# Optimization experiments

Hardware: AMD Instinct MI355X
Metric: run time of the kernel (lower is better)

Reference implementation:

```python
import jax, jax.numpy as jnp
import numpy as np

B, L, D = 2, 2048, 1024
H = 16
C = 128            # chunk_size
N = L // C         # num chunks
SCALE = float(np.sqrt(D))  # softmax_scale = sqrt(d_model)


def setup_inputs() -> dict:
    key = jax.random.key(0)
    ks = jax.random.split(key, 5)
    return {
        "x": jax.random.normal(ks[0], (B, L, D), dtype=jnp.float32),
        "w_qkv": jax.random.normal(ks[1], (D, 3 * D), dtype=jnp.float32) * (1.0 / np.sqrt(D)),
        "b_qkv": jax.random.normal(ks[2], (3 * D,), dtype=jnp.float32) * 0.02,
        "w_o": jax.random.normal(ks[3], (D, D), dtype=jnp.float32) * (1.0 / np.sqrt(D)),
        "b_o": jax.random.normal(ks[4], (D,), dtype=jnp.float32) * 0.02,
    }


def reference(x, w_qkv, b_qkv, w_o, b_o):
    b, l, d = x.shape
    hd = d // H
    qkv = x @ w_qkv + b_qkv                         # (B,L,3D)
    q, k, v = jnp.split(qkv, 3, axis=-1)
    q = q.reshape(b, l, H, hd)
    k = k.reshape(b, l, H, hd)
    v = v.reshape(b, l, H, hd)

    q_chunks = q.reshape(b, N, C, H, hd)
    k_chunks = k.reshape(b, N, C, H, hd)
    # mean_pool over the chunk dim
    q_pool = q_chunks.mean(axis=2)                  # (B,N,H,hd)
    k_pool = k_chunks.mean(axis=2)

    token2chunk = jnp.einsum('blhd,bnhd->bhln', q, k_pool)          # (B,H,L,N)
    chunk2token = jnp.einsum('bnhd,bnchd->bhnc', q_pool, k_chunks)  # (B,H,N,C)
    # outer product over (n,c) -> full (B,H,L,L) score matrix
    A = token2chunk[..., :, None] * chunk2token[:, :, None, :, :]   # (B,H,L,N,C)
    A = A.reshape(b, H, l, l)

    # direct intra-chunk attention overwrites the diagonal blocks
    direct = jnp.einsum('bnqhd,bnkhd->bhnqk', q_chunks, k_chunks)   # (B,H,N,C,C)
    A6 = A.reshape(b, H, N, C, N, C)
    eye = jnp.eye(N, dtype=bool)[:, None, :, None]                  # (N,1,N,1)
    A6 = jnp.where(eye, direct[:, :, :, :, None, :], A6)
    A = A6.reshape(b, H, l, l)

    # causal mask applied multiplicatively (masked scores become 0, NOT -inf)
    causal = jnp.tril(jnp.ones((l, l), dtype=bool))
    A = jnp.where(causal, A, 0.0) / SCALE
    A = jax.nn.softmax(A, axis=-1)

    out = jnp.einsum('bhqv,bvhd->bhqd', A, v)       # (B,H,L,hd)
    out = out.transpose(0, 2, 1, 3).reshape(b, l, d)
    return out @ w_o + b_o
```

## Files before the change

kernel.cpp:

```cpp
#include <hip/hip_runtime.h>
#include <math.h>

#define B_   2
#define L_   2048
#define D_   1024
#define H_   16
#define HD_  64
#define C_   128
#define N_   16
#define INV_SCALE 0.03125f
#define SCL2 0.0450842200f

typedef _Float16 h8 __attribute__((ext_vector_type(8)));
typedef _Float16 h4 __attribute__((ext_vector_type(4)));
typedef float    f4 __attribute__((ext_vector_type(4)));

#define MFMA16(a, b, c) __builtin_amdgcn_mfma_f32_16x16x32_f16((a), (b), (c), 0, 0, 0)

#if __has_builtin(__builtin_amdgcn_exp2f)
#define EXP2(x) __builtin_amdgcn_exp2f(x)
#else
#define EXP2(x) exp2f(x)
#endif

__device__ __forceinline__ void gl_lds16(const void* g, void* l) {
  __builtin_amdgcn_global_load_lds(
      (const __attribute__((address_space(1))) void*)g,
      (__attribute__((address_space(3))) void*)l, 16, 0, 0);
}

#define SBAR()  do { __builtin_amdgcn_sched_barrier(0); \
                     __builtin_amdgcn_s_barrier();      \
                     __builtin_amdgcn_sched_barrier(0); } while (0)
#define LGKM0() do { asm volatile("s_waitcnt lgkmcnt(0)" ::: "memory"); \
                     __builtin_amdgcn_sched_barrier(0); } while (0)
#define VMW(n)  do { asm volatile("s_waitcnt vmcnt(" #n ")" ::: "memory"); \
                     __builtin_amdgcn_sched_barrier(0); } while (0)

__global__ __launch_bounds__(256) void prep_kernel(
    const float* __restrict__ X, _Float16* __restrict__ Xh,
    const float* __restrict__ Wq, _Float16* __restrict__ WqT,
    const float* __restrict__ Wo, _Float16* __restrict__ WoT)
{
  __shared__ float ts[32][36];
  const int tid = threadIdx.x;
  const int id = blockIdx.x;
  if (id < 4096) {
    int i = id * 1024 + tid * 4;
    float4 v = *(const float4*)(X + i);
    h4 o = { (_Float16)v.x, (_Float16)v.y, (_Float16)v.z, (_Float16)v.w };
    *(h4*)(Xh + i) = o;
    return;
  }
  const float* W; _Float16* WT; int Nc, bx, by;
  if (id < 7168) {
    int idx = id - 4096;
    W = Wq; WT = WqT; Nc = 3072; bx = idx % 96; by = idx / 96;
  } else {
    int idx = id - 7168;
    W = Wo; WT = WoT; Nc = 1024; bx = idx & 31; by = idx >> 5;
  }
  const int n0 = bx * 32, k0 = by * 32;
  {
    int kr = tid >> 3, nc4 = (tid & 7) * 4;
    float4 v = *(const float4*)&W[(size_t)(k0 + kr) * Nc + n0 + nc4];
    ts[kr][nc4+0] = v.x; ts[kr][nc4+1] = v.y; ts[kr][nc4+2] = v.z; ts[kr][nc4+3] = v.w;
  }
  __syncthreads();
  {
    int nr = tid >> 3, kc4 = (tid & 7) * 4;
    h4 o = { (_Float16)ts[kc4+0][nr], (_Float16)ts[kc4+1][nr],
             (_Float16)ts[kc4+2][nr], (_Float16)ts[kc4+3][nr] };
    *(h4*)&WT[(size_t)(n0 + nr) * 1024 + k0 + kc4] = o;
  }
}

__global__ __launch_bounds__(512, 2) void qkv256_kernel(
    const _Float16* __restrict__ A, const _Float16* __restrict__ Bt,
    const float* __restrict__ bias,
    _Float16* __restrict__ Qh, _Float16* __restrict__ Kh, _Float16* __restrict__ VT,
    float* __restrict__ QP, float* __restrict__ KP, float* __restrict__ VCS)
{
  __shared__ __align__(16) _Float16 As[2][16384];
  __shared__ __align__(16) _Float16 Bs[2][12288];

  const int tid = threadIdx.x;
  const int w = tid >> 6, lane = tid & 63;
  const int q = lane >> 4, r = lane & 15, r7 = r & 7;
  const int wm = w >> 2, wn = w & 3;

  const int id = blockIdx.x, xcd = id & 7, slot = id >> 3;
  const int m0 = ((xcd >> 1) * 4 + (slot & 3)) * 256;
  const int n0 = ((xcd & 1) * 8 + (slot >> 2)) * 192;

  const int srow = tid >> 3;
  const int spart = (tid & 7) ^ (srow & 7);
  const _Float16* Asrc = A  + (size_t)(m0 + srow) * 1024 + spart * 8;
  const _Float16* Bsrc = Bt + (size_t)(n0 + srow) * 1024 + spart * 8;
  const int ldst = w * 512;

  const int aoffb = (wm * 128 + r) * 64;
  const int boffb = (wn * 48 + r) * 64;
  const int k0s = (q ^ r7) << 3;
  const int k1s = ((4 + q) ^ r7) << 3;

  auto stA = [&](int cc, int ko, int qq) {
    gl_lds16(Asrc + (size_t)qq * 65536 + ko, &As[cc][qq * 4096 + ldst]);
  };
  auto stB = [&](int cc, int ko, int qq) {
    gl_lds16(Bsrc + (size_t)qq * 65536 + ko, &Bs[cc][qq * 4096 + ldst]);
  };

  f4 acc[8][3];
  #pragma unroll
  for (int m = 0; m < 8; ++m)
    #pragma unroll
    for (int n = 0; n < 3; ++n) acc[m][n] = (f4){0.f, 0.f, 0.f, 0.f};

  stB(0, 0, 0); stB(0, 0, 1); stB(0, 0, 2);
  stA(0, 0, 0); stA(0, 0, 2); stA(0, 0, 1); stA(0, 0, 3);
  VMW(2);
  SBAR();

  for (int t = 0; t < 16; ++t) {
    const int c = t & 1;
    const _Float16* __restrict__ Ab = As[c];
    const _Float16* __restrict__ Bb = Bs[c];
    const int kt = (t + 1) << 6;
    const bool pf = (t < 15);
    h8 af[4], bf[3];

    #pragma unroll
    for (int m = 0; m < 4; ++m) af[m] = *(const h8*)&Ab[aoffb + m * 1024 + k0s];
    #pragma unroll
    for (int n = 0; n < 3; ++n) bf[n] = *(const h8*)&Bb[boffb + n * 1024 + k0s];
    if (pf) { stB(c ^ 1, kt, 0); stB(c ^ 1, kt, 1); stB(c ^ 1, kt, 2); }
    SBAR();
    LGKM0();
    __builtin_amdgcn_s_setprio(1);
    #pragma unroll
    for (int m = 0; m < 4; ++m)
      #pragma unroll
      for (int n = 0; n < 3; ++n) acc[m][n] = MFMA16(af[m], bf[n], acc[m][n]);
    __builtin_amdgcn_s_setprio(0);
    __builtin_amdgcn_sched_barrier(0);
    if (pf) { VMW(3); } else { VMW(0); }
    SBAR();

    #pragma unroll
    for (int m = 0; m < 4; ++m) af[m] = *(const h8*)&Ab[aoffb + (4 + m) * 1024 + k0s];
    if (pf) { stA(c ^ 1, kt, 0); stA(c ^ 1, kt, 2); stA(c ^ 1, kt, 1); }
    SBAR();
    LGKM0();
    __builtin_amdgcn_s_setprio(1);
    #pragma unroll
    for (int m = 0; m < 4; ++m)
      #pragma unroll
      for (int n = 0; n < 3; ++n) acc[4 + m][n] = MFMA16(af[m], bf[n], acc[4 + m][n]);
    __builtin_amdgcn_s_setprio(0);
    __builtin_amdgcn_sched_barrier(0);
    SBAR();

    #pragma unroll
    for (int m = 0; m < 4; ++m) af[m] = *(const h8*)&Ab[aoffb + m * 1024 + k1s];
    #pragma unroll
    for (int n = 0; n < 3; ++n) bf[n] = *(const h8*)&Bb[boffb + n * 1024 + k1s];
    if (pf) { stA(c ^ 1, kt, 3); }
    SBAR();
    LGKM0();
    __builtin_amdgcn_s_setprio(1);
    #pragma unroll
    for (int m = 0; m < 4; ++m)
      #pragma unroll
      for (int n = 0; n < 3; ++n) acc[m][n] = MFMA16(af[m], bf[n], acc[m][n]);
    __builtin_amdgcn_s_setprio(0);
    __builtin_amdgcn_sched_barrier(0);
    SBAR();

    #pragma unroll
    for (int m = 0; m < 4; ++m) af[m] = *(const h8*)&Ab[aoffb + (4 + m) * 1024 + k1s];
    if (pf) {
      VMW(2);
    }
    SBAR();
    LGKM0();
    __builtin_amdgcn_s_setprio(1);
    #pragma unroll
    for (int m = 0; m < 4; ++m)
      #pragma unroll
      for (int n = 0; n < 3; ++n) acc[4 + m][n] = MFMA16(af[m], bf[n], acc[4 + m][n]);
    __builtin_amdgcn_s_setprio(0);
    __builtin_amdgcn_sched_barrier(0);
    SBAR();
  }

  const int rb = m0 + wm * 128;
  const int b2 = rb >> 11;
  const int nch = (rb & 2047) >> 7;
  #pragma unroll
  for (int tc = 0; tc < 3; ++tc) {
    const int gn = n0 + wn * 48 + tc * 16 + r;
    const float bj = bias[gn];
    const int which = gn >> 10, rem = gn & 1023;
    const int h2 = rem >> 6, d2 = rem & 63;
    if (which < 2) {
      _Float16* dst = which == 0 ? Qh : Kh;
      #pragma unroll
      for (int m = 0; m < 8; ++m)
        #pragma unroll
        for (int i = 0; i < 4; ++i) {
          const int gm = rb + m * 16 + q * 4 + i;
          const int l2 = gm & 2047;
          dst[(((size_t)(b2 * H_ + h2)) * L_ + l2) * HD_ + d2] =
              (_Float16)(acc[m][tc][i] + bj);
        }
    } else {
      #pragma unroll
      for (int m = 0; m < 8; ++m) {
        const int gm0 = rb + m * 16 + q * 4;
        const int l2 = gm0 & 2047;
        h4 hv = { (_Float16)(acc[m][tc][0] + bj), (_Float16)(acc[m][tc][1] + bj),
                  (_Float16)(acc[m][tc][2] + bj), (_Float16)(acc[m][tc][3] + bj) };
        *(h4*)&VT[((size_t)(b2 * H_ + h2) * HD_ + d2) * L_ + l2] = hv;
      }
    }
    float s2 = 0.f;
    #pragma unroll
    for (int m = 0; m < 8; ++m)
      #pragma unroll
      for (int i = 0; i < 4; ++i) s2 += acc[m][tc][i];
    s2 += __shfl_xor(s2, 16);
    s2 += __shfl_xor(s2, 32);
    if (q == 0) {
      const size_t o = (((size_t)(b2 * H_ + h2)) * N_ + nch) * HD_ + d2;
      if (which == 0)      QP[o] = s2 * (1.f / 128.f) + bj;
      else if (which == 1) KP[o] = s2 * (1.f / 128.f) + bj;
      else                 VCS[o] = s2 + 128.f * bj;
    }
  }
}

template<int MT>
__global__ __launch_bounds__(256, 4) void gemm16_kernel(
    const _Float16* __restrict__ A, const _Float16* __restrict__ Bt,
    const float* __restrict__ bias, float* __restrict__ out, int Kd)
{
  constexpr int SM = MT / 32;
  __shared__ __align__(16) _Float16 As[2][MT * 32];
  __shared__ __align__(16) _Float16 Bs[2][4096];
  const int tid = threadIdx.x;
  const int lane = tid & 63, w = tid >> 6;
  const int q = lane >> 4, r = lane & 15;
  const int mb = (w >> 1) * (MT / 2);
  const int nb = (w & 1) * 64;

  int m0, n0;
  {
    const int id = blockIdx.x;
    const int xcd = id & 7, slot = id >> 3;
    m0 = (xcd * 8 + (slot >> 3)) * 64;
    n0 = (slot & 7) * 128;
  }

  const int Rr = tid >> 2;
  const int cd = (tid & 3) ^ ((Rr >> 1) & 3);
  const _Float16* Ag = A + (size_t)(m0 + Rr) * Kd + cd * 8;
  const _Float16* Bg = Bt + (size_t)(n0 + Rr) * Kd + cd * 8;
  const size_t rowStep = (size_t)64 * Kd;

  f4 acc[SM][4];
  #pragma unroll
  for (int s = 0; s < SM; ++s)
    #pragma unroll
    for (int t = 0; t < 4; ++t) acc[s][t] = (f4){0.f, 0.f, 0.f, 0.f};

  const int nIter = Kd >> 5;
  const int koff = (q ^ ((r >> 1) & 3)) << 3;

  auto stage = [&](int bf, int kt) {
    _Float16* Asl = &As[bf][w * 512];
    _Float16* Bsl = &Bs[bf][w * 512];
    gl_lds16(Ag + kt, Asl);
    if constexpr (MT == 128) gl_lds16(Ag + kt + rowStep, Asl + 2048);
    gl_lds16(Bg + kt, Bsl);
    gl_lds16(Bg + kt + rowStep, Bsl + 2048);
  };

  stage(0, 0);

  for (int it = 0; it < nIter; ++it) {
    __syncthreads();
    if (it + 1 < nIter) stage((it + 1) & 1, (it + 1) << 5);
    const _Float16* Ab = As[it & 1];
    const _Float16* Bb = Bs[it & 1];
    h8 af[SM], bf4[4];
    #pragma unroll
    for (int s = 0; s < SM; ++s)
      af[s] = *(const h8*)&Ab[(mb + s * 16 + r) * 32 + koff];
    #pragma unroll
    for (int t = 0; t < 4; ++t)
      bf4[t] = *(const h8*)&Bb[(nb + t * 16 + r) * 32 + koff];
    #pragma unroll
    for (int s = 0; s < SM; ++s)
      #pragma unroll
      for (int t = 0; t < 4; ++t)
        acc[s][t] = MFMA16(af[s], bf4[t], acc[s][t]);
  }

  #pragma unroll
  for (int t = 0; t < 4; ++t) {
    int gn = n0 + nb + t * 16 + r;
    float bj = bias[gn];
    #pragma unroll
    for (int s = 0; s < SM; ++s)
      #pragma unroll
      for (int i = 0; i < 4; ++i) {
        int gm = m0 + mb + s * 16 + q * 4 + i;
        out[(size_t)gm * 1024 + gn] = acc[s][t][i] + bj;
      }
  }
}

__global__ __launch_bounds__(128) void pool2_kernel(
    const float* __restrict__ QP, const _Float16* __restrict__ Kh,
    const float* __restrict__ VCS,
    float* __restrict__ C2T, float* __restrict__ C2TMX, float* __restrict__ C2TMN,
    float* __restrict__ CSUF)
{
  __shared__ float qp_s[64];
  __shared__ float red[4];
  if (blockIdx.x >= 512) {
    int bh = blockIdx.x - 512, d = threadIdx.x;
    if (d < 64) {
      float run = 0.f;
      for (int n = N_ - 1; n >= 0; --n) {
        size_t o = ((size_t)bh * N_ + n) * HD_ + d;
        CSUF[o] = run;
        run += VCS[o];
      }
    }
    return;
  }
  int bh = blockIdx.x >> 4, n = blockIdx.x & 15, tid = threadIdx.x;
  int w = tid >> 6, lane = tid & 63;
  if (tid < 64) qp_s[tid] = QP[((size_t)bh * N_ + n) * HD_ + tid];
  const _Float16* kr = Kh + (((size_t)bh * L_) + n * C_ + tid) * HD_;
  h8 kv[8];
  #pragma unroll
  for (int c8 = 0; c8 < 8; ++c8) kv[c8] = *(const h8*)(kr + c8 * 8);
  __syncthreads();
  float s = 0.f;
  #pragma unroll
  for (int c8 = 0; c8 < 8; ++c8)
    #pragma unroll
    for (int j = 0; j < 8; ++j)
      s = fmaf((float)kv[c8][j], qp_s[c8 * 8 + j], s);
  C2T[((size_t)bh * N_ + n) * C_ + tid] = s;
  float mx = s, mn = s;
  #pragma unroll
  for (int st = 1; st <= 32; st <<= 1) {
    mx = fmaxf(mx, __shfl_xor(mx, st));
    mn = fminf(mn, __shfl_xor(mn, st));
  }
  if (lane == 0) { red[w * 2] = mx; red[w * 2 + 1] = mn; }
  __syncthreads();
  if (tid == 0) {
    C2TMX[bh * N_ + n] = fmaxf(red[0], red[2]);
    C2TMN[bh * N_ + n] = fminf(red[1], red[3]);
  }
}

__global__ __launch_bounds__(512, 4) void attn4_kernel(
    const _Float16* __restrict__ Qh, const _Float16* __restrict__ Kh,
    const _Float16* __restrict__ VT,
    const float* __restrict__ C2T, const float* __restrict__ C2TMX,
    const float* __restrict__ C2TMN, const float* __restrict__ CSUF,
    const float* __restrict__ KP, _Float16* __restrict__ AOh)
{
  __shared__ __align__(16) _Float16 buf0[8192];
  __shared__ __align__(16) _Float16 buf1[8192];
  __shared__ __align__(16) _Float16 buf2[8192];
  __shared__ __align__(16) _Float16 kp_s[1024];
  __shared__ __align__(16) float c2t_s[2][128];

  const int tid = threadIdx.x;
  const int w = tid >> 6, lane = tid & 63;
  const int q = lane >> 4, r = lane & 15;
  const int r7 = r & 7;
  const int id = blockIdx.x;
  const int bh = ((id & 7) << 2) + ((id >> 3) & 3);
  const int s5 = id >> 5;
  const int nq = (s5 < 8) ? (15 - s5) : (s5 - 8);
  const int l0 = nq * 128;
  const int rowA = l0 + w * 16 + r;
  const int pcw = w * 16 + r;
  const size_t bhL = (size_t)bh * L_;
  const int b2 = bh >> 4, h2 = bh & 15;

  auto stageV = [&](_Float16* buf, int n) {
    #pragma unroll
    for (int j2 = 0; j2 < 2; ++j2) {
      int f = j2 * 512 + tid;
      int d = f >> 4, p = f & 15;
      int c16 = p ^ (d & 7);
      gl_lds16(VT + ((size_t)bh * HD_ + d) * L_ + n * C_ + c16 * 8,
               buf + (size_t)(j2 * 512 + w * 64) * 8);
    }
  };
  auto stageK = [&](_Float16* buf, int n) {
    #pragma unroll
    for (int j2 = 0; j2 < 2; ++j2) {
      int f = j2 * 512 + tid;
      int c = f >> 3, p = f & 7;
      int ck = p ^ (c & 7);
      gl_lds16(Kh + (bhL + n * C_ + c) * HD_ + ck * 8,
               buf + (size_t)(j2 * 512 + w * 64) * 8);
    }
  };
  auto stageC = [&](int bf, int n) {
    if (tid < 32)
      gl_lds16(C2T + ((size_t)bh * N_ + n) * C_ + tid * 4, &c2t_s[bf][0]);
  };

  if (tid < 256) {
    int n4 = tid >> 4, d4 = (tid & 15) * 4;
    float4 kpv = *(const float4*)&KP[((size_t)bh * N_ + n4) * HD_ + d4];
    int sd = ((((d4 >> 3) ^ (n4 & 7)) << 3) | (d4 & 7));
    h4 hv = { (_Float16)kpv.x, (_Float16)kpv.y, (_Float16)kpv.z, (_Float16)kpv.w };
    *(h4*)&kp_s[n4 * 64 + sd] = hv;
  }
  h8 qa0 = *(const h8*)(Qh + (bhL + rowA) * HD_ + q * 8);
  h8 qa1 = *(const h8*)(Qh + (bhL + rowA) * HD_ + 32 + q * 8);
  float mxL = C2TMX[bh * N_ + r];
  float mnL = C2TMN[bh * N_ + r];
  stageK(buf0, nq);
  stageV(buf2, nq);
  if (nq >= 1) stageC(0, nq - 1);
  __syncthreads();

  f4 tvacc = (f4){0.f, 0.f, 0.f, 0.f};
  {
    h8 kpa0 = *(const h8*)&kp_s[r * 64 + ((q ^ r7) << 3)];
    h8 kpa1 = *(const h8*)&kp_s[r * 64 + (((4 + q) ^ r7) << 3)];
    tvacc = MFMA16(kpa0, qa0, tvacc);
    tvacc = MFMA16(kpa1, qa1, tvacc);
  }
  float tvs[4];
  #pragma unroll
  for (int i = 0; i < 4; ++i) tvs[i] = tvacc[i] * SCL2;

  float pm = -1e30f;
  #pragma unroll
  for (int i = 0; i < 4; ++i) {
    int n = q * 4 + i;
    float mx = __shfl(mxL, n);
    float mn = __shfl(mnL, n);
    float cm = fmaxf(tvs[i] * mx, tvs[i] * mn);
    pm = (n < nq) ? fmaxf(pm, cm) : pm;
  }
  pm = fmaxf(pm, __shfl_xor(pm, 16));
  pm = fmaxf(pm, __shfl_xor(pm, 32));

  f4 sc[8];
  #pragma unroll
  for (int u = 0; u < 8; ++u) sc[u] = (f4){0.f, 0.f, 0.f, 0.f};
  {
    h8 kc0 = *(const h8*)&buf0[r * 64 + ((q ^ r7) << 3)];
    h8 kc1 = *(const h8*)&buf0[r * 64 + (((4 + q) ^ r7) << 3)];
    #pragma unroll
    for (int u = 0; u < 8; ++u) {
      h8 kn0, kn1;
      if (u < 7) {
        kn0 = *(const h8*)&buf0[((u + 1) * 16 + r) * 64 + ((q ^ r7) << 3)];
        kn1 = *(const h8*)&buf0[((u + 1) * 16 + r) * 64 + (((4 + q) ^ r7) << 3)];
      }
      sc[u] = MFMA16(kc0, qa0, sc[u]);
      sc[u] = MFMA16(kc1, qa1, sc[u]);
      kc0 = kn0; kc1 = kn1;
    }
  }

  float rm = -1e30f;
  #pragma unroll
  for (int u = 0; u < 8; ++u)
    #pragma unroll
    for (int i = 0; i < 4; ++i) {
      int lcol = u * 16 + q * 4 + i;
      float v = sc[u][i] * SCL2;
      v = (lcol <= pcw) ? v : -1e30f;
      sc[u][i] = v;
      rm = fmaxf(rm, v);
    }
  rm = fmaxf(rm, __shfl_xor(rm, 16));
  rm = fmaxf(rm, __shfl_xor(rm, 32));

  const float M = fmaxf(fmaxf(pm, rm), 0.f);
  const float e0 = EXP2(-M);

  __syncthreads();

  _Float16* pw = (w < 4) ? (buf0 + w * 2048) : (buf1 + (w - 4) * 2048);
  const int pwbase = r * 128 + ((q & 1) << 2);
  float csl = 0.f;
  #pragma unroll
  for (int u = 0; u < 8; ++u) {
    h4 pv4;
    #pragma unroll
    for (int i = 0; i < 4; ++i) {
      float v = sc[u][i];
      float p = (v > -1e29f) ? EXP2(v - M) : 0.f;
      csl += p;
      pv4[i] = (_Float16)p;
    }
    *(h4*)&pw[pwbase + ((((u << 1) | (q >> 1)) ^ r7) << 3)] = pv4;
  }
  csl += __shfl_xor(csl, 16);
  csl += __shfl_xor(csl, 32);
  float den = csl;

  f4 oacc[4], sacc[4];
  #pragma unroll
  for (int t = 0; t < 4; ++t) {
    oacc[t] = (f4){0.f, 0.f, 0.f, 0.f};
    sacc[t] = (f4){0.f, 0.f, 0.f, 0.f};
  }
  {
    h8 pcur = *(const h8*)&pw[r * 128 + ((q ^ r7) << 3)];
    h8 vcur[4];
    #pragma unroll
    for (int t = 0; t < 4; ++t)
      vcur[t] = *(const h8*)&buf2[(t * 16 + r) * 128 + ((q ^ r7) << 3)];
    #pragma unroll
    for (int s = 0; s < 4; ++s) {
      h8 pnxt; h8 vnxt[4];
      if (s < 3) {
        pnxt = *(const h8*)&pw[r * 128 + ((((s + 1) * 4 + q) ^ r7) << 3)];
        #pragma unroll
        for (int t = 0; t < 4; ++t)
          vnxt[t] = *(const h8*)&buf2[(t * 16 + r) * 128 + ((((s + 1) * 4 + q) ^ r7) << 3)];
      }
      h8 mk;
      #pragma unroll
      for (int j2 = 0; j2 < 8; ++j2)
        mk[j2] = (_Float16)((s * 32 + q * 8 + j2 > pcw) ? 1.f : 0.f);
      #pragma unroll
      for (int t = 0; t < 4; ++t) {
        oacc[t] = MFMA16(pcur, vcur[t], oacc[t]);
        sacc[t] = MFMA16(mk, vcur[t], sacc[t]);
      }
      pcur = pnxt;
      #pragma unroll
      for (int t = 0; t < 4; ++t) vcur[t] = vnxt[t];
    }
  }

  __syncthreads();
  if (nq >= 1) stageV(buf1, nq - 1);

  float dsum = 0.f;
  const float negM = -M;
  for (int n = nq - 1; n >= 0; --n) {
    const int k = nq - 1 - n;
    const _Float16* curb = (k & 1) ? buf2 : buf1;
    __syncthreads();
    if (n >= 1) {
      stageV((k & 1) ? buf1 : buf2, n - 1);
      stageC((k + 1) & 1, n - 1);
    }
    int i0 = n & 3;
    float tvx = i0 == 0 ? tvs[0] : i0 == 1 ? tvs[1] : i0 == 2 ? tvs[2] : tvs[3];
    float tvn = __shfl(tvx, ((n >> 2) << 4) + r);
    const float* c2p = c2t_s[k & 1];

    f4 cca = *(const f4*)&c2p[q * 8];
    f4 ccb = *(const f4*)&c2p[q * 8 + 4];
    h8 vcur[4];
    #pragma unroll
    for (int t = 0; t < 4; ++t)
      vcur[t] = *(const h8*)&curb[(t * 16 + r) * 128 + ((q ^ r7) << 3)];

    #pragma unroll
    for (int s = 0; s < 4; ++s) {
      f4 can, cbn; h8 vnxt[4];
      if (s < 3) {
        can = *(const f4*)&c2p[(s + 1) * 32 + q * 8];
        cbn = *(const f4*)&c2p[(s + 1) * 32 + q * 8 + 4];
        #pragma unroll
        for (int t = 0; t < 4; ++t)
          vnxt[t] = *(const h8*)&curb[(t * 16 + r) * 128 + ((((s + 1) * 4 + q) ^ r7) << 3)];
      }
      float p0 = EXP2(fmaf(tvn, cca[0], negM)), p1 = EXP2(fmaf(tvn, cca[1], negM));
      float p2 = EXP2(fmaf(tvn, cca[2], negM)), p3 = EXP2(fmaf(tvn, cca[3], negM));
      float p4 = EXP2(fmaf(tvn, ccb[0], negM)), p5 = EXP2(fmaf(tvn, ccb[1], negM));
      float p6 = EXP2(fmaf(tvn, ccb[2], negM)), p7 = EXP2(fmaf(tvn, ccb[3], negM));
      dsum += p0 + p1 + p2 + p3 + p4 + p5 + p6 + p7;
      h8 pa = { (_Float16)p0, (_Float16)p1, (_Float16)p2, (_Float16)p3,
                (_Float16)p4, (_Float16)p5, (_Float16)p6, (_Float16)p7 };
      #pragma unroll
      for (int t = 0; t < 4; ++t)
        oacc[t] = MFMA16(pa, vcur[t], oacc[t]);
      cca = can; ccb = cbn;
      #pragma unroll
      for (int t = 0; t < 4; ++t) vcur[t] = vnxt[t];
    }
  }
  dsum += __shfl_xor(dsum, 16);
  dsum += __shfl_xor(dsum, 32);
  den += dsum;

  int cnt = (L_ - 1) - rowA;
  den += e0 * (float)cnt;
  float e0r[4], dnr[4];
  #pragma unroll
  for (int i = 0; i < 4; ++i) {
    e0r[i] = __shfl(e0,  (q << 2) + i);
    dnr[i] = __shfl(den, (q << 2) + i);
  }
  #pragma unroll
  for (int t = 0; t < 4; ++t) {
    int d = t * 16 + r;
    float csf = CSUF[((size_t)bh * N_ + nq) * HD_ + d];
    #pragma unroll
    for (int i = 0; i < 4; ++i) {
      int row = l0 + w * 16 + q * 4 + i;
      float suffix = sacc[t][i] + csf;
      float o = (oacc[t][i] + e0r[i] * suffix) / dnr[i];
      AOh[((size_t)b2 * L_ + row) * D_ + h2 * HD_ + d] = (_Float16)o;
    }
  }
}

extern "C" void kernel_launch(void* const* d_in, const int* in_sizes, int n_in,
                              void* d_out, int out_size, void* d_ws, size_t ws_size,
                              hipStream_t stream)
{
  (void)in_sizes; (void)n_in; (void)out_size; (void)ws_size;
  const float* x     = (const float*)d_in[0];
  const float* w_qkv = (const float*)d_in[1];
  const float* b_qkv = (const float*)d_in[2];
  const float* w_o   = (const float*)d_in[3];
  const float* b_o   = (const float*)d_in[4];
  float* out = (float*)d_out;

  char* p = (char*)d_ws;
  _Float16* xh   = (_Float16*)p; p += (size_t)4194304 * 2;
  _Float16* wqT  = (_Float16*)p; p += (size_t)3145728 * 2;
  _Float16* woT  = (_Float16*)p; p += (size_t)1048576 * 2;
  _Float16* Qh   = (_Float16*)p; p += (size_t)4194304 * 2;
  _Float16* Kh   = (_Float16*)p; p += (size_t)4194304 * 2;
  _Float16* VT   = (_Float16*)p; p += (size_t)4194304 * 2;
  _Float16* AOh  = (_Float16*)p; p += (size_t)4194304 * 2;
  float*    C2T  = (float*)p;    p += (size_t)65536 * 4;
  float*    QP   = (float*)p;    p += (size_t)32768 * 4;
  float*    KP   = (float*)p;    p += (size_t)32768 * 4;
  float*    VCS  = (float*)p;    p += (size_t)32768 * 4;
  float*    CSUF = (float*)p;    p += (size_t)32768 * 4;
  float*    MXa  = (float*)p;    p += (size_t)512 * 4;
  float*    MNa  = (float*)p;    p += (size_t)512 * 4;

  prep_kernel<<<8192, 256, 0, stream>>>(x, xh, w_qkv, wqT, w_o, woT);
  qkv256_kernel<<<256, 512, 0, stream>>>(
      xh, wqT, b_qkv, Qh, Kh, VT, QP, KP, VCS);
  pool2_kernel<<<544, 128, 0, stream>>>(QP, Kh, VCS, C2T, MXa, MNa, CSUF);
  attn4_kernel<<<512, 512, 0, stream>>>(
      Qh, Kh, VT, C2T, MXa, MNa, CSUF, KP, AOh);
  gemm16_kernel<64><<<512, 256, 0, stream>>>(
      AOh, woT, b_o, out, D_);
}
```

Baseline: 168.7 us.

## Drop LDS staging in attention kernel and read K, V, C2T directly from global

After: 218.5 us. +29.5%, slower.

```diff
diff --git a/kernel.cpp b/kernel.cpp
--- a/kernel.cpp
+++ b/kernel.cpp
@@ -283,7 +283,8 @@
     gl_lds16(Ag + kt, Asl);
     if constexpr (MT == 128) gl_lds16(Ag + kt + rowStep, Asl + 2048);
     gl_lds16(Bg + kt, Bsl);
-    gl_lds16(Bg + kt + rowStep, Bsl + 2048);
+    if constexpr (MT == 128) gl_lds16(Bg + kt + rowStep, Bsl + 2048);
+    else gl_lds16(Bg + kt + rowStep, Bsl + 2048);
   };
 
   stage(0, 0);
@@ -370,18 +371,14 @@
   }
 }
 
-__global__ __launch_bounds__(512, 4) void attn4_kernel(
+__global__ __launch_bounds__(512, 4) void attn6_kernel(
     const _Float16* __restrict__ Qh, const _Float16* __restrict__ Kh,
     const _Float16* __restrict__ VT,
     const float* __restrict__ C2T, const float* __restrict__ C2TMX,
     const float* __restrict__ C2TMN, const float* __restrict__ CSUF,
     const float* __restrict__ KP, _Float16* __restrict__ AOh)
 {
-  __shared__ __align__(16) _Float16 buf0[8192];
-  __shared__ __align__(16) _Float16 buf1[8192];
-  __shared__ __align__(16) _Float16 buf2[8192];
-  __shared__ __align__(16) _Float16 kp_s[1024];
-  __shared__ __align__(16) float c2t_s[2][128];
+  __shared__ __align__(16) _Float16 pwb[16384];
 
   const int tid = threadIdx.x;
   const int w = tid >> 6, lane = tid & 63;
@@ -397,51 +394,22 @@
   const size_t bhL = (size_t)bh * L_;
   const int b2 = bh >> 4, h2 = bh & 15;
 
-  auto stageV = [&](_Float16* buf, int n) {
-    #pragma unroll
-    for (int j2 = 0; j2 < 2; ++j2) {
-      int f = j2 * 512 + tid;
-      int d = f >> 4, p = f & 15;
-      int c16 = p ^ (d & 7);
-      gl_lds16(VT + ((size_t)bh * HD_ + d) * L_ + n * C_ + c16 * 8,
-               buf + (size_t)(j2 * 512 + w * 64) * 8);
-    }
-  };
-  auto stageK = [&](_Float16* buf, int n) {
-    #pragma unroll
-    for (int j2 = 0; j2 < 2; ++j2) {
-      int f = j2 * 512 + tid;
-      int c = f >> 3, p = f & 7;
-      int ck = p ^ (c & 7);
-      gl_lds16(Kh + (bhL + n * C_ + c) * HD_ + ck * 8,
-               buf + (size_t)(j2 * 512 + w * 64) * 8);
-    }
-  };
-  auto stageC = [&](int bf, int n) {
-    if (tid < 32)
-      gl_lds16(C2T + ((size_t)bh * N_ + n) * C_ + tid * 4, &c2t_s[bf][0]);
-  };
-
-  if (tid < 256) {
-    int n4 = tid >> 4, d4 = (tid & 15) * 4;
-    float4 kpv = *(const float4*)&KP[((size_t)bh * N_ + n4) * HD_ + d4];
-    int sd = ((((d4 >> 3) ^ (n4 & 7)) << 3) | (d4 & 7));
-    h4 hv = { (_Float16)kpv.x, (_Float16)kpv.y, (_Float16)kpv.z, (_Float16)kpv.w };
-    *(h4*)&kp_s[n4 * 64 + sd] = hv;
-  }
   h8 qa0 = *(const h8*)(Qh + (bhL + rowA) * HD_ + q * 8);
   h8 qa1 = *(const h8*)(Qh + (bhL + rowA) * HD_ + 32 + q * 8);
   float mxL = C2TMX[bh * N_ + r];
   float mnL = C2TMN[bh * N_ + r];
-  stageK(buf0, nq);
-  stageV(buf2, nq);
-  if (nq >= 1) stageC(0, nq - 1);
-  __syncthreads();
 
   f4 tvacc = (f4){0.f, 0.f, 0.f, 0.f};
   {
-    h8 kpa0 = *(const h8*)&kp_s[r * 64 + ((q ^ r7) << 3)];
-    h8 kpa1 = *(const h8*)&kp_s[r * 64 + (((4 + q) ^ r7) << 3)];
+    const float* kp0 = KP + ((size_t)bh * N_ + r) * HD_ + q * 8;
+    float4 a0 = *(const float4*)(kp0);
+    float4 a1 = *(const float4*)(kp0 + 4);
+    float4 c0 = *(const float4*)(kp0 + 32);
+    float4 c1 = *(const float4*)(kp0 + 36);
+    h8 kpa0 = { (_Float16)a0.x, (_Float16)a0.y, (_Float16)a0.z, (_Float16)a0.w,
+                (_Float16)a1.x, (_Float16)a1.y, (_Float16)a1.z, (_Float16)a1.w };
+    h8 kpa1 = { (_Float16)c0.x, (_Float16)c0.y, (_Float16)c0.z, (_Float16)c0.w,
+                (_Float16)c1.x, (_Float16)c1.y, (_Float16)c1.z, (_Float16)c1.w };
     tvacc = MFMA16(kpa0, qa0, tvacc);
     tvacc = MFMA16(kpa1, qa1, tvacc);
   }
@@ -465,18 +433,13 @@
   #pragma unroll
   for (int u = 0; u < 8; ++u) sc[u] = (f4){0.f, 0.f, 0.f, 0.f};
   {
-    h8 kc0 = *(const h8*)&buf0[r * 64 + ((q ^ r7) << 3)];
-    h8 kc1 = *(const h8*)&buf0[r * 64 + (((4 + q) ^ r7) << 3)];
+    const _Float16* kbase = Kh + (bhL + l0 + r) * HD_ + q * 8;
     #pragma unroll
     for (int u = 0; u < 8; ++u) {
-      h8 kn0, kn1;
-      if (u < 7) {
-        kn0 = *(const h8*)&buf0[((u + 1) * 16 + r) * 64 + ((q ^ r7) << 3)];
-        kn1 = *(const h8*)&buf0[((u + 1) * 16 + r) * 64 + (((4 + q) ^ r7) << 3)];
-      }
+      h8 kc0 = *(const h8*)(kbase + u * 16 * HD_);
+      h8 kc1 = *(const h8*)(kbase + u * 16 * HD_ + 32);
       sc[u] = MFMA16(kc0, qa0, sc[u]);
       sc[u] = MFMA16(kc1, qa1, sc[u]);
-      kc0 = kn0; kc1 = kn1;
     }
   }
 
@@ -497,9 +460,7 @@
   const float M = fmaxf(fmaxf(pm, rm), 0.f);
   const float e0 = EXP2(-M);
 
-  __syncthreads();
-
-  _Float16* pw = (w < 4) ? (buf0 + w * 2048) : (buf1 + (w - 4) * 2048);
+  _Float16* pw = pwb + w * 2048;
   const int pwbase = r * 128 + ((q & 1) << 2);
   float csl = 0.f;
   #pragma unroll
@@ -524,71 +485,35 @@
     oacc[t] = (f4){0.f, 0.f, 0.f, 0.f};
     sacc[t] = (f4){0.f, 0.f, 0.f, 0.f};
   }
-  {
-    h8 pcur = *(const h8*)&pw[r * 128 + ((q ^ r7) << 3)];
-    h8 vcur[4];
-    #pragma unroll
-    for (int t = 0; t < 4; ++t)
-      vcur[t] = *(const h8*)&buf2[(t * 16 + r) * 128 + ((q ^ r7) << 3)];
-    #pragma unroll
-    for (int s = 0; s < 4; ++s) {
-      h8 pnxt; h8 vnxt[4];
-      if (s < 3) {
-        pnxt = *(const h8*)&pw[r * 128 + ((((s + 1) * 4 + q) ^ r7) << 3)];
-        #pragma unroll
-        for (int t = 0; t < 4; ++t)
-          vnxt[t] = *(const h8*)&buf2[(t * 16 + r) * 128 + ((((s + 1) * 4 + q) ^ r7) << 3)];
-      }
-      h8 mk;
-      #pragma unroll
-      for (int j2 = 0; j2 < 8; ++j2)
-        mk[j2] = (_Float16)((s * 32 + q * 8 + j2 > pcw) ? 1.f : 0.f);
-      #pragma unroll
-      for (int t = 0; t < 4; ++t) {
-        oacc[t] = MFMA16(pcur, vcur[t], oacc[t]);
-        sacc[t] = MFMA16(mk, vcur[t], sacc[t]);
-      }
-      pcur = pnxt;
-      #pragma unroll
-      for (int t = 0; t < 4; ++t) vcur[t] = vnxt[t];
-    }
-  }
-
-  __syncthreads();
-  if (nq >= 1) stageV(buf1, nq - 1);
+  #pragma unroll
+  for (int s = 0; s < 4; ++s) {
+    h8 pa = *(const h8*)&pw[r * 128 + (((s * 4 + q) ^ r7) << 3)];
+    h8 mk;
+    #pragma unroll
+    for (int j2 = 0; j2 < 8; ++j2)
+      mk[j2] = (_Float16)((s * 32 + q * 8 + j2 > pcw) ? 1.f : 0.f);
+    #pragma unroll
+    for (int t = 0; t < 4; ++t) {
+      h8 vb = *(const h8*)(VT + ((size_t)bh * HD_ + t * 16 + r) * L_ +
+                           l0 + s * 32 + q * 8);
+      oacc[t] = MFMA16(pa, vb, oacc[t]);
+      sacc[t] = MFMA16(mk, vb, sacc[t]);
+    }
+  }
 
   float dsum = 0.f;
   const float negM = -M;
   for (int n = nq - 1; n >= 0; --n) {
-    const int k = nq - 1 - n;
-    const _Float16* curb = (k & 1) ? buf2 : buf1;
-    __syncthreads();
-    if (n >= 1) {
-      stageV((k & 1) ? buf1 : buf2, n - 1);
-      stageC((k + 1) & 1, n - 1);
-    }
     int i0 = n & 3;
     float tvx = i0 == 0 ? tvs[0] : i0 == 1 ? tvs[1] : i0 == 2 ? tvs[2] : tvs[3];
     float tvn = __shfl(tvx, ((n >> 2) << 4) + r);
-    const float* c2p = c2t_s[k & 1];
-
-    f4 cca = *(const f4*)&c2p[q * 8];
-    f4 ccb = *(const f4*)&c2p[q * 8 + 4];
-    h8 vcur[4];
-    #pragma unroll
-    for (int t = 0; t < 4; ++t)
-      vcur[t] = *(const h8*)&curb[(t * 16 + r) * 128 + ((q ^ r7) << 3)];
+    const float* c2p = C2T + ((size_t)bh * N_ + n) * C_;
+    const _Float16* vrow = VT + (size_t)bh * HD_ * L_ + n * C_;
 
     #pragma unroll
     for (int s = 0; s < 4; ++s) {
-      f4 can, cbn; h8 vnxt[4];
-      if (s < 3) {
-        can = *(const f4*)&c2p[(s + 1) * 32 + q * 8];
-        cbn = *(const f4*)&c2p[(s + 1) * 32 + q * 8 + 4];
-        #pragma unroll
-        for (int t = 0; t < 4; ++t)
-          vnxt[t] = *(const h8*)&curb[(t * 16 + r) * 128 + ((((s + 1) * 4 + q) ^ r7) << 3)];
-      }
+      f4 cca = *(const f4*)(c2p + s * 32 + q * 8);
+      f4 ccb = *(const f4*)(c2p + s * 32 + q * 8 + 4);
       float p0 = EXP2(fmaf(tvn, cca[0], negM)), p1 = EXP2(fmaf(tvn, cca[1], negM));
       float p2 = EXP2(fmaf(tvn, cca[2], negM)), p3 = EXP2(fmaf(tvn, cca[3], negM));
       float p4 = EXP2(fmaf(tvn, ccb[0], negM)), p5 = EXP2(fmaf(tvn, ccb[1], negM));
@@ -597,11 +522,11 @@
       h8 pa = { (_Float16)p0, (_Float16)p1, (_Float16)p2, (_Float16)p3,
                 (_Float16)p4, (_Float16)p5, (_Float16)p6, (_Float16)p7 };
       #pragma unroll
-      for (int t = 0; t < 4; ++t)
-        oacc[t] = MFMA16(pa, vcur[t], oacc[t]);
-      cca = can; ccb = cbn;
-      #pragma unroll
-      for (int t = 0; t < 4; ++t) vcur[t] = vnxt[t];
+      for (int t = 0; t < 4; ++t) {
+        h8 vb = *(const h8*)(vrow + ((size_t)(t * 16 + r)) * L_ +
+                             s * 32 + q * 8);
+        oacc[t] = MFMA16(pa, vb, oacc[t]);
+      }
     }
   }
   dsum += __shfl_xor(dsum, 16);
@@ -662,7 +587,7 @@
   qkv256_kernel<<<256, 512, 0, stream>>>(
       xh, wqT, b_qkv, Qh, Kh, VT, QP, KP, VCS);
   pool2_kernel<<<544, 128, 0, stream>>>(QP, Kh, VCS, C2T, MXa, MNa, CSUF);
-  attn4_kernel<<<512, 512, 0, stream>>>(
+  attn6_kernel<<<512, 512, 0, stream>>>(
       Qh, Kh, VT, C2T, MXa, MNa, CSUF, KP, AOh);
   gemm16_kernel<64><<<512, 256, 0, stream>>>(
       AOh, woT, b_o, out, D_);
```
